# Kernel optimization log

Hardware: AMD Instinct MI355X
Metric: run time of the kernel (lower is better)

Reference implementation:

```python
import jax, jax.numpy as jnp
import numpy as np


def setup_inputs() -> dict:
    key = jax.random.key(0)
    k1, k2 = jax.random.split(key)
    x = jax.random.normal(k1, (4, 1, 16384), dtype=jnp.float32)  # [B, C, T]
    # dictionary initialized uniform(-1, 1) as in nn.Parameter(...).uniform_(-1, 1)
    d = jax.random.uniform(k2, (256, 1, 256), dtype=jnp.float32, minval=-1.0, maxval=1.0)  # [A, C, K]
    return {"x": x, "d": d, "n_iterations": 16}


def reference(x, d, n_iterations):
    B, C, T = x.shape
    A, _, K = d.shape
    pad = K // 2
    # normalize each atom over (channels, atom_size) dims, i.e. d_normalization_dims=(-1,-2)
    norms = jnp.linalg.norm(d.reshape(A, -1), axis=-1)
    dn = d / (norms[:, None, None] + 1e-12)

    # work in a padded domain so conv output position == start index in padded residual
    rp = jnp.pad(x, ((0, 0), (0, 0), (pad, pad)))        # residual, [B, C, T+2*pad]
    recon = jnp.zeros_like(rp)                            # accumulated reconstruction
    Tout = T + 2 * pad - K + 1                            # conv output length

    def step(carry, _):
        rp, recon = carry
        # cross-correlation of residual with every atom: [B, A, Tout]
        fm = jax.lax.conv_general_dilated(
            rp, dn, window_strides=(1,), padding='VALID',
            dimension_numbers=('NCH', 'OIH', 'NCH'))
        flat = fm.reshape(B, A * Tout)
        idx = jnp.argmax(flat, axis=-1)                   # signed max, per batch item
        val = jnp.take_along_axis(flat, idx[:, None], axis=-1)[:, 0]
        atom_idx = idx // Tout
        pos = idx % Tout                                  # start index in padded domain
        atoms = dn[atom_idx] * val[:, None, None]         # [B, C, K]

        def upd(r, rec, a, p):
            seg = jax.lax.dynamic_slice(r, (0, p), (C, K))
            r2 = jax.lax.dynamic_update_slice(r, seg - a, (0, p))
            segr = jax.lax.dynamic_slice(rec, (0, p), (C, K))
            rec2 = jax.lax.dynamic_update_slice(rec, segr + a, (0, p))
            return r2, rec2

        rp2, recon2 = jax.vmap(upd)(rp, recon, atoms, pos)
        return (rp2, recon2), None

    (rp, recon), _ = jax.lax.scan(step, (rp, recon), None, length=n_iterations)
    # crop padding -> reconstruction with same shape as x
    return recon[:, :, pad:pad + T]
```

## Files before the change

kernel.cpp:

```cpp
#include <hip/hip_runtime.h>
#include <math.h>

#define B    4
#define T    16384
#define A    256
#define K    256
#define PAD  128
#define TP   (T + 2*PAD)
#define TOUT (TP - K + 1)
#define ITERS 16
#define CHUNK 512
#define NCHUNK 33
#define NCP  36
#define TILE 2048
#define NTILE 9
#define NBLK 512
#define BPB2 128
#define HBASE 8192
#define RPSTORE 8448
#define RPN 8704
#define NGRP 8
#define SUBSTRIDE 32
#define BARSTRIDE (NGRP*SUBSTRIDE)
#define DLDS 40960

#define TAP(acc, s0,s1,s2,s3, dq) { acc = fmaf(s0,(dq).x,acc); acc = fmaf(s1,(dq).y,acc); \
                                    acc = fmaf(s2,(dq).z,acc); acc = fmaf(s3,(dq).w,acc); }

typedef unsigned long long u64;

__device__ __forceinline__ void wave_amax(float& bv, int& bi) {
    #pragma unroll
    for (int off = 32; off; off >>= 1) {
        float ov = __shfl_down(bv, off);
        int   oi = __shfl_down(bi, off);
        if (ov > bv || (ov == bv && oi < bi)) { bv = ov; bi = oi; }
    }
}

struct KSmem {
    float  rp[RPN];
    float4 dn4[4][64];
    float  chv[4][34];
    int    chi[4][34];
    float  wv[16]; int wi[16];
    float  fv; int fi;
};

__device__ __forceinline__ void gbar_sub(unsigned* sub, int r, unsigned gen16, int tid) {
    __syncthreads();
    if (tid == 0)
        __hip_atomic_fetch_add(&sub[(r >> 4)*SUBSTRIDE], 1u,
                               __ATOMIC_RELEASE, __HIP_MEMORY_SCOPE_AGENT);
    if (tid < 64) {
        for (;;) {
            unsigned ok = 1;
            if (tid < NGRP)
                ok = (__hip_atomic_load(&sub[tid*SUBSTRIDE], __ATOMIC_RELAXED,
                                        __HIP_MEMORY_SCOPE_AGENT) >= gen16);
            if (__all((int)ok)) break;
            __builtin_amdgcn_s_sleep(4);
        }
    }
    __syncthreads();
    __builtin_amdgcn_fence(__ATOMIC_ACQUIRE, "agent");
}

__device__ void chunks_update(KSmem& sm, int baseF, int cA, int cB, int aBase, int tid) {
    const int lane = tid & 63, w = tid >> 6;
    const int grp = tid >> 7;
    const int cg = grp ? cB : cA;
    const int lt = cg*512 + (tid & 127)*4;
    float c0[4] = {0,0,0,0}, c1[4] = {0,0,0,0}, c2[4] = {0,0,0,0}, c3[4] = {0,0,0,0};
    if (cg >= 0) {
        const float4* srp4 = (const float4*)sm.rp;
        int ol4 = (lt - baseF) >> 2;
        float4 p = srp4[ol4];
        #pragma unroll 4
        for (int kq = 0; kq < 64; kq++) {
            float4 d0 = sm.dn4[0][kq];
            float4 d1 = sm.dn4[1][kq];
            float4 d2 = sm.dn4[2][kq];
            float4 d3 = sm.dn4[3][kq];
            float4 pn = srp4[ol4 + kq + 1];
            TAP(c0[0], p.x,p.y,p.z,p.w, d0); TAP(c0[1], p.y,p.z,p.w,pn.x, d0);
            TAP(c0[2], p.z,p.w,pn.x,pn.y, d0); TAP(c0[3], p.w,pn.x,pn.y,pn.z, d0);
            TAP(c1[0], p.x,p.y,p.z,p.w, d1); TAP(c1[1], p.y,p.z,p.w,pn.x, d1);
            TAP(c1[2], p.z,p.w,pn.x,pn.y, d1); TAP(c1[3], p.w,pn.x,pn.y,pn.z, d1);
            TAP(c2[0], p.x,p.y,p.z,p.w, d2); TAP(c2[1], p.y,p.z,p.w,pn.x, d2);
            TAP(c2[2], p.z,p.w,pn.x,pn.y, d2); TAP(c2[3], p.w,pn.x,pn.y,pn.z, d2);
            TAP(c3[0], p.x,p.y,p.z,p.w, d3); TAP(c3[1], p.y,p.z,p.w,pn.x, d3);
            TAP(c3[2], p.z,p.w,pn.x,pn.y, d3); TAP(c3[3], p.w,pn.x,pn.y,pn.z, d3);
            p = pn;
        }
    }
    float bv0 = -INFINITY, bv1 = -INFINITY, bv2 = -INFINITY, bv3 = -INFINITY;
    int bi0 = 0x7fffffff, bi1 = 0x7fffffff, bi2 = 0x7fffffff, bi3 = 0x7fffffff;
    if (cg >= 0) {
        #pragma unroll
        for (int j = 0; j < 4; j++) {
            int t = lt + j;
            if (t < TOUT) {
                if (c0[j] > bv0) { bv0 = c0[j]; bi0 = (aBase+0)*TOUT + t; }
                if (c1[j] > bv1) { bv1 = c1[j]; bi1 = (aBase+1)*TOUT + t; }
                if (c2[j] > bv2) { bv2 = c2[j]; bi2 = (aBase+2)*TOUT + t; }
                if (c3[j] > bv3) { bv3 = c3[j]; bi3 = (aBase+3)*TOUT + t; }
            }
        }
    }
    wave_amax(bv0, bi0); wave_amax(bv1, bi1); wave_amax(bv2, bi2); wave_amax(bv3, bi3);
    if (lane == 0) {
        sm.wv[0*4+w] = bv0; sm.wi[0*4+w] = bi0;
        sm.wv[1*4+w] = bv1; sm.wi[1*4+w] = bi1;
        sm.wv[2*4+w] = bv2; sm.wi[2*4+w] = bi2;
        sm.wv[3*4+w] = bv3; sm.wi[3*4+w] = bi3;
    }
    __syncthreads();
    if (tid < 8) {
        int a = tid >> 1, hh = tid & 1;
        int chunk = hh ? cB : cA;
        if (chunk >= 0) {
            float v0 = sm.wv[a*4 + 2*hh];   int i0 = sm.wi[a*4 + 2*hh];
            float v1 = sm.wv[a*4 + 2*hh+1]; int i1 = sm.wi[a*4 + 2*hh+1];
            if (v1 > v0 || (v1 == v0 && i1 < i0)) { v0 = v1; i0 = i1; }
            sm.chv[a][chunk] = v0; sm.chi[a][chunk] = i0;
        }
    }
    __syncthreads();
}

__device__ __forceinline__ void slot_write(KSmem& sm, u64* wp, int gen, int h, int tid) {
    const int lane = tid & 63, w = tid >> 6;
    int cstart = h ? 16 : 0, nch = h ? 17 : 16;
    float bv = -INFINITY; int bi = 0x7fffffff;
    if (lane < nch) { bv = sm.chv[w][cstart + lane]; bi = sm.chi[w][cstart + lane]; }
    wave_amax(bv, bi);
    if (lane == 0) { sm.wv[8+w] = bv; sm.wi[8+w] = bi; }
    __syncthreads();
    if (tid == 0) {
        float v = sm.wv[8]; int i = sm.wi[8];
        #pragma unroll
        for (int j = 1; j < 4; j++)
            if (sm.wv[8+j] > v || (sm.wv[8+j] == v && sm.wi[8+j] < i)) { v = sm.wv[8+j]; i = sm.wi[8+j]; }
        u64 e = ((u64)(unsigned)(gen + 1) << 56)
              | ((u64)__float_as_uint(v) << 24)
              | (u64)(unsigned)i;
        __hip_atomic_store(wp, e, __ATOMIC_RELAXED, __HIP_MEMORY_SCOPE_AGENT);
    }
}

__device__ __forceinline__ void pick_poll(KSmem& sm, const u64* sl, int gen, int tid) {
    const int lane = tid & 63, w = tid >> 6;
    float v = -INFINITY; int i = 0x7fffffff;
    if (tid < BPB2) {
        const u64* p = sl + tid;
        u64 e;
        for (;;) {
            e = __hip_atomic_load(p, __ATOMIC_RELAXED, __HIP_MEMORY_SCOPE_AGENT);
            if ((unsigned)(e >> 56) == (unsigned)(gen + 1)) break;
            __builtin_amdgcn_s_sleep(1);
        }
        v = __uint_as_float((unsigned)((e >> 24) & 0xFFFFFFFFull));
        i = (int)(e & 0x7FFFFF);
    }
    if (w < 2) {
        wave_amax(v, i);
        if (lane == 0) { sm.wv[w] = v; sm.wi[w] = i; }
    }
    __syncthreads();
    if (tid == 0) {
        float bv = sm.wv[0]; int bi = sm.wi[0];
        if (sm.wv[1] > bv || (sm.wv[1] == bv && sm.wi[1] < bi)) { bv = sm.wv[1]; bi = sm.wi[1]; }
        sm.fv = bv; sm.fi = bi;
    }
    __syncthreads();
}

__global__ void __launch_bounds__(256, 2)
k_coop(const float* __restrict__ x, const float* __restrict__ d, float* __restrict__ out,
       float* __restrict__ dn, u64* __restrict__ slots, unsigned* __restrict__ bar) {
    extern __shared__ char raw[];
    KSmem& sm = *(KSmem*)raw;
    const int bid = blockIdx.x, tid = threadIdx.x;
    const int b = bid >> 7, r = bid & 127;
    const int h = r >> 6, a0 = r & 63;
    const int lane = tid & 63, w = tid >> 6;
    const int baseF = h * HBASE;
    const int cstart = h ? 16 : 0, cend = h ? 33 : 16;
    u64* slotsb = slots + (size_t)b*2*BPB2;
    unsigned* sub = bar + b*BARSTRIDE;

    {
        const float4* x4 = (const float4*)(x + (size_t)b*T);
        float4* rp4w = (float4*)sm.rp;
        int b4 = baseF >> 2;
        for (int i = tid; i < RPN/4; i += 256) {
            int g4 = b4 + i;
            float4 v = {0.f,0.f,0.f,0.f};
            if (i < RPSTORE/4 && g4 >= PAD/4 && g4 < (PAD+T)/4) v = x4[g4 - PAD/4];
            rp4w[i] = v;
        }
    }
    #pragma unroll
    for (int s = 0; s < 4; s++) {
        int atom = a0*4 + s;
        float v = d[atom*K + tid];
        float sq = v*v;
        #pragma unroll
        for (int off = 32; off; off >>= 1) sq += __shfl_down(sq, off);
        if (lane == 0) sm.wv[w] = sq;
        __syncthreads();
        float norm = sqrtf(sm.wv[0] + sm.wv[1] + sm.wv[2] + sm.wv[3]) + 1e-12f;
        float nv = v / norm;
        ((float*)&sm.dn4[s][0])[tid] = nv;
        dn[atom*K + tid] = nv;
        __syncthreads();
    }
    {
        int npass = h ? 9 : 8;
        for (int p = 0; p < npass; p++) {
            int ca = cstart + 2*p;
            int cb2 = (ca + 1 < cend) ? ca + 1 : -1;
            chunks_update(sm, baseF, ca, cb2, a0*4, tid);
        }
    }
    slot_write(sm, slotsb + 0*BPB2 + r, 0, h, tid);
    gbar_sub(sub, r, 16u, tid);

    for (int it = 0; it < ITERS-1; it++) {
        pick_poll(sm, slotsb + (it & 1)*BPB2, it, tid);
        float val = sm.fv; int idx = sm.fi;
        int atom = idx / TOUT, pos = idx - atom*TOUT;
        float ds = dn[atom*K + tid];
        int li = pos + tid - baseF;
        if (li >= 0 && li < RPSTORE) sm.rp[li] -= val * ds;
        __syncthreads();
        int lo = pos - (K-1); if (lo < 0) lo = 0;
        int g0 = lo >> 9, g1 = g0 + 1;
        bool in0 = (g0 >= cstart && g0 < cend);
        bool in1 = (g1 >= cstart && g1 < cend);
        int ca = in0 ? g0 : (in1 ? g1 : -1);
        int cb2 = (in0 && in1) ? g1 : -1;
        if (ca >= 0) chunks_update(sm, baseF, ca, cb2, a0*4, tid);
        slot_write(sm, slotsb + ((it+1) & 1)*BPB2 + r, it+1, h, tid);
    }
    if (a0 == 0) {
        pick_poll(sm, slotsb + ((ITERS-1) & 1)*BPB2, ITERS-1, tid);
        float val = sm.fv; int idx = sm.fi;
        int atom = idx / TOUT, pos = idx - atom*TOUT;
        float ds = dn[atom*K + tid];
        int li = pos + tid - baseF;
        if (li >= 0 && li < RPSTORE) sm.rp[li] -= val * ds;
        __syncthreads();
        int o_lo4 = h ? (HBASE - PAD)/4 : 0;
        int o_hi4 = h ? T/4 : (HBASE - PAD)/4;
        const float4* xb4 = (const float4*)(x + (size_t)b*T);
        float4* o4 = (float4*)(out + (size_t)b*T);
        for (int i4 = o_lo4 + tid; i4 < o_hi4; i4 += 256) {
            float4 xv = xb4[i4];
            float4 rv = *(const float4*)&sm.rp[i4*4 + PAD - baseF];
            float4 ov; ov.x = xv.x - rv.x; ov.y = xv.y - rv.y;
            ov.z = xv.z - rv.z; ov.w = xv.w - rv.w;
            o4[i4] = ov;
        }
    }
}

struct Smem {
    float rp[TILE + K + 16];
    float dnA[K];
    float dnB[K];
    float dnsel[K];
    float wv[16]; int wi[16];
    float fv; int fi;
};

__device__ __forceinline__ void dev_norm(int a0, int tid, const float* __restrict__ d,
                                         float* __restrict__ dn, Smem& sm) {
    int lane = tid & 63, w = tid >> 6;
    #pragma unroll
    for (int s = 0; s < 2; s++) {
        int atom = a0*2 + s;
        float v = d[atom*K + tid];
        float sq = v*v;
        #pragma unroll
        for (int off = 32; off; off >>= 1) sq += __shfl_down(sq, off);
        if (lane == 0) sm.wv[w] = sq;
        __syncthreads();
        float norm = sqrtf(sm.wv[0] + sm.wv[1] + sm.wv[2] + sm.wv[3]) + 1e-12f;
        dn[atom*K + tid] = v / norm;
        __syncthreads();
    }
}

__device__ __forceinline__ void dev_init(int a0, int b, int tid, const float* __restrict__ x,
                                         float* __restrict__ rp, float* __restrict__ recon) {
    int i = a0*256 + tid;
    if (i < TP) {
        float v = (i >= PAD && i < PAD + T) ? x[b*T + (i - PAD)] : 0.f;
        rp[(size_t)b*TP + i] = v;
        recon[(size_t)b*TP + i] = 0.f;
    }
}

__device__ void dev_conv(int a0, int b, int tid, const float* __restrict__ rp,
                         const float* __restrict__ dn,
                         float* __restrict__ segval, int* __restrict__ segidx,
                         float* __restrict__ abv, int* __restrict__ abi, Smem& sm) {
    const int aA = a0*2, aB = a0*2 + 1;
    const int lane = tid & 63, w = tid >> 6;
    sm.dnA[tid] = dn[aA*K + tid];
    sm.dnB[tid] = dn[aB*K + tid];
    const float4* rp4 = (const float4*)(rp + (size_t)b*TP);

    for (int tile = 0; tile < NTILE; tile++) {
        int t0 = tile * TILE;
        __syncthreads();
        float4* s4 = (float4*)sm.rp;
        for (int i = tid; i < 580; i += 256) {
            int g = t0/4 + i;
            float4 v = {0.f,0.f,0.f,0.f};
            if (g*4 < TP) v = rp4[g];
            s4[i] = v;
        }
        __syncthreads();
        const float4* srp4 = (const float4*)sm.rp;
        const float4* dA4  = (const float4*)sm.dnA;
        const float4* dB4  = (const float4*)sm.dnB;
        float accA0[4] = {0,0,0,0}, accA1[4] = {0,0,0,0};
        float accB0[4] = {0,0,0,0}, accB1[4] = {0,0,0,0};
        float4 p = srp4[tid];
        float4 q = srp4[tid + 256];
        #pragma unroll 4
        for (int kq = 0; kq < 64; kq++) {
            float4 dA = dA4[kq];
            float4 dB = dB4[kq];
            float4 pn = srp4[tid + kq + 1];
            float4 qn = srp4[tid + 256 + kq + 1];
            TAP(accA0[0], p.x,p.y,p.z,p.w, dA); TAP(accA0[1], p.y,p.z,p.w,pn.x, dA);
            TAP(accA0[2], p.z,p.w,pn.x,pn.y, dA); TAP(accA0[3], p.w,pn.x,pn.y,pn.z, dA);
            TAP(accB0[0], p.x,p.y,p.z,p.w, dB); TAP(accB0[1], p.y,p.z,p.w,pn.x, dB);
            TAP(accB0[2], p.z,p.w,pn.x,pn.y, dB); TAP(accB0[3], p.w,pn.x,pn.y,pn.z, dB);
            TAP(accA1[0], q.x,q.y,q.z,q.w, dA); TAP(accA1[1], q.y,q.z,q.w,qn.x, dA);
            TAP(accA1[2], q.z,q.w,qn.x,qn.y, dA); TAP(accA1[3], q.w,qn.x,qn.y,qn.z, dA);
            TAP(accB1[0], q.x,q.y,q.z,q.w, dB); TAP(accB1[1], q.y,q.z,q.w,qn.x, dB);
            TAP(accB1[2], q.z,q.w,qn.x,qn.y, dB); TAP(accB1[3], q.w,qn.x,qn.y,qn.z, dB);
            p = pn; q = qn;
        }
        int lt = tid * 4;
        float bvA0 = -INFINITY, bvA1 = -INFINITY, bvB0 = -INFINITY, bvB1 = -INFINITY;
        int biA0 = 0x7fffffff, biA1 = 0x7fffffff, biB0 = 0x7fffffff, biB1 = 0x7fffffff;
        #pragma unroll
        for (int j = 0; j < 4; j++) {
            int t = t0 + lt + j;
            if (t < TOUT) {
                if (accA0[j] > bvA0) { bvA0 = accA0[j]; biA0 = aA*TOUT + t; }
                if (accB0[j] > bvB0) { bvB0 = accB0[j]; biB0 = aB*TOUT + t; }
            }
            int t1 = t0 + 1024 + lt + j;
            if (t1 < TOUT) {
                if (accA1[j] > bvA1) { bvA1 = accA1[j]; biA1 = aA*TOUT + t1; }
                if (accB1[j] > bvB1) { bvB1 = accB1[j]; biB1 = aB*TOUT + t1; }
            }
        }
        wave_amax(bvA0, biA0); wave_amax(bvA1, biA1);
        wave_amax(bvB0, biB0); wave_amax(bvB1, biB1);
        if (lane == 0) {
            sm.wv[w]    = bvA0; sm.wi[w]    = biA0;
            sm.wv[4+w]  = bvA1; sm.wi[4+w]  = biA1;
            sm.wv[8+w]  = bvB0; sm.wi[8+w]  = biB0;
            sm.wv[12+w] = bvB1; sm.wi[12+w] = biB1;
        }
        __syncthreads();
        if (tid < 4) {
            float v0 = sm.wv[2*tid];   int i0 = sm.wi[2*tid];
            float v1 = sm.wv[2*tid+1]; int i1 = sm.wi[2*tid+1];
            if (v1 > v0 || (v1 == v0 && i1 < i0)) { v0 = v1; i0 = i1; }
            int chunk = tile*4 + tid;
            if (chunk < NCHUNK) {
                segval[((size_t)b*A + aA)*NCP + chunk] = v0;
                segidx[((size_t)b*A + aA)*NCP + chunk] = i0;
            }
        } else if (tid >= 64 && tid < 68) {
            int c = tid - 64;
            float v0 = sm.wv[8+2*c];   int i0 = sm.wi[8+2*c];
            float v1 = sm.wv[8+2*c+1]; int i1 = sm.wi[8+2*c+1];
            if (v1 > v0 || (v1 == v0 && i1 < i0)) { v0 = v1; i0 = i1; }
            int chunk = tile*4 + c;
            if (chunk < NCHUNK) {
                segval[((size_t)b*A + aB)*NCP + chunk] = v0;
                segidx[((size_t)b*A + aB)*NCP + chunk] = i0;
            }
        }
    }
    __syncthreads();
    if (w < 2) {
        int atom = (w == 0) ? aA : aB;
        float bv = -INFINITY; int bi = 0x7fffffff;
        if (lane < NCHUNK) {
            bv = segval[((size_t)b*A + atom)*NCP + lane];
            bi = segidx[((size_t)b*A + atom)*NCP + lane];
        }
        wave_amax(bv, bi);
        if (lane == 0) { abv[b*A + atom] = bv; abi[b*A + atom] = bi; }
    }
}

__device__ void dev_iter(int a0, int b, int tid, int last,
                         const float* __restrict__ avc, const int* __restrict__ aic,
                         float* __restrict__ avn, int* __restrict__ ain,
                         const float* __restrict__ rin, float* __restrict__ rout,
                         float* __restrict__ recon, const float* __restrict__ dn,
                         float* __restrict__ segval, int* __restrict__ segidx, Smem& sm) {
    const int aA = a0*2, aB = a0*2 + 1;
    const int lane = tid & 63, w = tid >> 6;

    float bv0 = avc[b*A + tid]; int bi0 = aic[b*A + tid];
    const float4* rin4 = (const float4*)(rin + (size_t)b*TP);
    const int icopy = a0*256 + tid;
    const bool docopy = (!last) && (icopy < TP/4);
    float4 vcopy = {0.f,0.f,0.f,0.f};
    if (docopy) vcopy = rin4[icopy];
    sm.dnA[tid] = dn[aA*K + tid];
    sm.dnB[tid] = dn[aB*K + tid];

    {
        float bv = bv0; int bi = bi0;
        wave_amax(bv, bi);
        if (lane == 0) { sm.wv[w] = bv; sm.wi[w] = bi; }
        __syncthreads();
        if (tid == 0) {
            bv = sm.wv[0]; bi = sm.wi[0];
            for (int j = 1; j < 4; j++)
                if (sm.wv[j] > bv || (sm.wv[j] == bv && sm.wi[j] < bi)) { bv = sm.wv[j]; bi = sm.wi[j]; }
            sm.fv = bv; sm.fi = bi;
        }
        __syncthreads();
    }
    float val = sm.fv; int idx = sm.fi;
    int atom = idx / TOUT, pos = idx - atom*TOUT;
    sm.dnsel[tid] = dn[atom*K + tid];

    int lo = pos - (K-1); if (lo < 0) lo = 0;
    int c_lo = lo >> 9;
    int tbase = c_lo * CHUNK;

    if (!last) {
        float4* s4 = (float4*)sm.rp;
        for (int i = tid; i < 324; i += 256) {
            int g = tbase/4 + i;
            float4 v = {0.f,0.f,0.f,0.f};
            if (g*4 < TP) v = rin4[g];
            s4[i] = v;
        }
    }
    __syncthreads();
    if (docopy) {
        float4* rout4 = (float4*)(rout + (size_t)b*TP);
        float4 v = vcopy;
        int o = icopy*4 - pos;
        if (o > -4 && o < K) {
            if (o+0 >= 0 && o+0 < K) v.x -= val * sm.dnsel[o+0];
            if (o+1 >= 0 && o+1 < K) v.y -= val * sm.dnsel[o+1];
            if (o+2 >= 0 && o+2 < K) v.z -= val * sm.dnsel[o+2];
            if (o+3 >= 0 && o+3 < K) v.w -= val * sm.dnsel[o+3];
        }
        rout4[icopy] = v;
    }
    if (a0 == 0) {
        recon[(size_t)b*TP + pos + tid] += val * sm.dnsel[tid];
    }
    if (last) return;

    sm.rp[pos + tid - tbase] -= val * sm.dnsel[tid];
    __syncthreads();

    const float4* srp4 = (const float4*)sm.rp;
    const float4* dA4  = (const float4*)sm.dnA;
    const float4* dB4  = (const float4*)sm.dnB;
    float cA[4] = {0,0,0,0}, cB[4] = {0,0,0,0};
    float4 p = srp4[tid];
    #pragma unroll 4
    for (int kq = 0; kq < 64; kq++) {
        float4 dA = dA4[kq];
        float4 dB = dB4[kq];
        float4 pn = srp4[tid + kq + 1];
        TAP(cA[0], p.x,p.y,p.z,p.w, dA); TAP(cA[1], p.y,p.z,p.w,pn.x, dA);
        TAP(cA[2], p.z,p.w,pn.x,pn.y, dA); TAP(cA[3], p.w,pn.x,pn.y,pn.z, dA);
        TAP(cB[0], p.x,p.y,p.z,p.w, dB); TAP(cB[1], p.y,p.z,p.w,pn.x, dB);
        TAP(cB[2], p.z,p.w,pn.x,pn.y, dB); TAP(cB[3], p.w,pn.x,pn.y,pn.z, dB);
        p = pn;
    }
    int lt = tid * 4;
    float bvA = -INFINITY, bvB = -INFINITY;
    int biA = 0x7fffffff, biB = 0x7fffffff;
    #pragma unroll
    for (int j = 0; j < 4; j++) {
        int t = tbase + lt + j;
        if (t < TOUT) {
            if (cA[j] > bvA) { bvA = cA[j]; biA = aA*TOUT + t; }
            if (cB[j] > bvB) { bvB = cB[j]; biB = aB*TOUT + t; }
        }
    }
    wave_amax(bvA, biA); wave_amax(bvB, biB);
    if (lane == 0) { sm.wv[w] = bvA; sm.wi[w] = biA; sm.wv[8+w] = bvB; sm.wi[8+w] = biB; }
    __syncthreads();
    if (tid < 2) {
        float v0 = sm.wv[2*tid];   int i0 = sm.wi[2*tid];
        float v1 = sm.wv[2*tid+1]; int i1 = sm.wi[2*tid+1];
        if (v1 > v0 || (v1 == v0 && i1 < i0)) { v0 = v1; i0 = i1; }
        int chunk = c_lo + tid;
        if (chunk < NCHUNK) {
            segval[((size_t)b*A + aA)*NCP + chunk] = v0;
            segidx[((size_t)b*A + aA)*NCP + chunk] = i0;
        }
    } else if (tid >= 64 && tid < 66) {
        int c = tid - 64;
        float v0 = sm.wv[8+2*c];   int i0 = sm.wi[8+2*c];
        float v1 = sm.wv[8+2*c+1]; int i1 = sm.wi[8+2*c+1];
        if (v1 > v0 || (v1 == v0 && i1 < i0)) { v0 = v1; i0 = i1; }
        int chunk = c_lo + c;
        if (chunk < NCHUNK) {
            segval[((size_t)b*A + aB)*NCP + chunk] = v0;
            segidx[((size_t)b*A + aB)*NCP + chunk] = i0;
        }
    }
    __syncthreads();
    if (w < 2) {
        int at = (w == 0) ? aA : aB;
        float bv = -INFINITY; int bi = 0x7fffffff;
        if (lane < NCHUNK) {
            bv = segval[((size_t)b*A + at)*NCP + lane];
            bi = segidx[((size_t)b*A + at)*NCP + lane];
        }
        wave_amax(bv, bi);
        if (lane == 0) { avn[b*A + at] = bv; ain[b*A + at] = bi; }
    }
}

__global__ void __launch_bounds__(256) k_f_norm_init(const float* x, const float* d,
                                                     float* dn, float* rp0, float* recon) {
    __shared__ Smem sm;
    dev_norm(blockIdx.x & 127, threadIdx.x, d, dn, sm);
    dev_init(blockIdx.x & 127, blockIdx.x >> 7, threadIdx.x, x, rp0, recon);
}
__global__ void __launch_bounds__(256, 2) k_f_conv(const float* rp, const float* dn,
                                                   float* segval, int* segidx,
                                                   float* abv, int* abi) {
    __shared__ Smem sm;
    dev_conv(blockIdx.x & 127, blockIdx.x >> 7, threadIdx.x, rp, dn, segval, segidx, abv, abi, sm);
}
__global__ void __launch_bounds__(256, 2) k_f_iter(int last,
                                                   const float* avc, const int* aic,
                                                   float* avn, int* ain,
                                                   const float* rin, float* rout,
                                                   float* recon, const float* dn,
                                                   float* segval, int* segidx) {
    __shared__ Smem sm;
    dev_iter(blockIdx.x & 127, blockIdx.x >> 7, threadIdx.x, last,
             avc, aic, avn, ain, rin, rout, recon, dn, segval, segidx, sm);
}
__global__ void k_f_out(const float* recon, float* out) {
    int i = blockIdx.x * blockDim.x + threadIdx.x;
    if (i >= B*T) return;
    int b = i / T, t = i - b*T;
    out[i] = recon[(size_t)b*TP + PAD + t];
}

extern "C" void kernel_launch(void* const* d_in, const int* in_sizes, int n_in,
                              void* d_out, int out_size, void* d_ws, size_t ws_size,
                              hipStream_t stream) {
    const float* x = (const float*)d_in[0];
    const float* d = (const float*)d_in[1];
    float* out = (float*)d_out;

    float* ws     = (float*)d_ws;
    float* dn     = ws;
    float* rp0    = dn  + (size_t)A*K;
    float* rp1    = rp0 + (size_t)B*TP;
    float* recon  = rp1 + (size_t)B*TP;
    float* segval = recon + (size_t)B*TP;
    int*   segidx = (int*)(segval + (size_t)B*A*NCP);
    float* abv0   = (float*)(segidx + (size_t)B*A*NCP);
    float* abv1   = abv0 + (size_t)B*2*A;
    int*   abi0   = (int*)(abv1 + (size_t)B*2*A);
    int*   abi1   = abi0 + (size_t)B*2*A;
    unsigned* bar = (unsigned*)(abi1 + (size_t)B*2*A);
    u64*  slots   = (u64*)(bar + (size_t)B*BARSTRIDE);

    (void)hipFuncSetAttribute((const void*)k_coop,
                              hipFuncAttributeMaxDynamicSharedMemorySize, DLDS);
    int nb = 0, ncu = 0;
    hipError_t e1 = hipOccupancyMaxActiveBlocksPerMultiprocessor(&nb, (const void*)k_coop,
                                                                 256, DLDS);
    hipError_t e2 = hipDeviceGetAttribute(&ncu, hipDeviceAttributeMultiprocessorCount, 0);
    bool coop = (e1 == hipSuccess && e2 == hipSuccess && nb > 0 && ncu > 0 &&
                 (long)nb * ncu >= NBLK);
    if (coop) {
        (void)hipMemsetAsync(bar, 0, B*BARSTRIDE*sizeof(unsigned), stream);
        (void)hipMemsetAsync(slots, 0xFF, (size_t)B*2*BPB2*sizeof(u64), stream);
        hipLaunchKernelGGL(k_coop, dim3(NBLK), dim3(256), DLDS, stream,
                           x, d, out, dn, slots, bar);
        return;
    }
    k_f_norm_init<<<NBLK, 256, 0, stream>>>(x, d, dn, rp0, recon);
    k_f_conv<<<NBLK, 256, 0, stream>>>(rp0, dn, segval, segidx, abv0, abi0);
    float* rbuf[2] = {rp0, rp1};
    float* av[2]   = {abv0, abv1};
    int*   ai[2]   = {abi0, abi1};
    for (int it = 0; it < ITERS; it++) {
        k_f_iter<<<NBLK, 256, 0, stream>>>(it == ITERS-1 ? 1 : 0,
                                           av[it & 1], ai[it & 1],
                                           av[(it + 1) & 1], ai[(it + 1) & 1],
                                           rbuf[it & 1], rbuf[(it + 1) & 1],
                                           recon, dn, segval, segidx);
    }
    k_f_out<<<(B*T + 255)/256, 256, 0, stream>>>(recon, out);
}
```

Baseline: 517.0 us.

## Replace per-block slot polling with grouped atomic-max argmax and arrival counters

Each block now folds its local best value and index into an order-preserving 64-bit key and does an atomic fetch_max into one of 8 group slots, then bumps a per-group arrival counter. Readers poll 8 counters and 8 group slots instead of 128 per-block slots, which shrinks polling traffic and the final reduction to a short shuffle. The generation is encoded in the high bits and slots are double-buffered by parity. Costs are atomic contention on shared slots and an explicit vmcnt wait between the max and the counter increment.

Result: no change. 517.0 us (-0.0%).

```diff
diff --git a/kernel.cpp b/kernel.cpp
--- a/kernel.cpp
+++ b/kernel.cpp
@@ -22,6 +22,8 @@
 #define NGRP 8
 #define SUBSTRIDE 32
 #define BARSTRIDE (NGRP*SUBSTRIDE)
+#define GSTRIDE 16
+#define GPAR (NGRP*GSTRIDE)
 #define DLDS 40960
 
 #define TAP(acc, s0,s1,s2,s3, dq) { acc = fmaf(s0,(dq).x,acc); acc = fmaf(s1,(dq).y,acc); \
@@ -129,7 +131,8 @@
     __syncthreads();
 }
 
-__device__ __forceinline__ void slot_write(KSmem& sm, u64* wp, int gen, int h, int tid) {
+__device__ __forceinline__ void publish(KSmem& sm, u64* gslot, unsigned* gcnt,
+                                        int gen, int h, int tid) {
     const int lane = tid & 63, w = tid >> 6;
     int cstart = h ? 16 : 0, nch = h ? 17 : 16;
     float bv = -INFINITY; int bi = 0x7fffffff;
@@ -142,43 +145,56 @@
         #pragma unroll
         for (int j = 1; j < 4; j++)
             if (sm.wv[8+j] > v || (sm.wv[8+j] == v && sm.wi[8+j] < i)) { v = sm.wv[8+j]; i = sm.wi[8+j]; }
-        u64 e = ((u64)(unsigned)(gen + 1) << 56)
-              | ((u64)__float_as_uint(v) << 24)
-              | (u64)(unsigned)i;
-        __hip_atomic_store(wp, e, __ATOMIC_RELAXED, __HIP_MEMORY_SCOPE_AGENT);
-    }
-}
-
-__device__ __forceinline__ void pick_poll(KSmem& sm, const u64* sl, int gen, int tid) {
-    const int lane = tid & 63, w = tid >> 6;
-    float v = -INFINITY; int i = 0x7fffffff;
-    if (tid < BPB2) {
-        const u64* p = sl + tid;
-        u64 e;
+        unsigned s = __float_as_uint(v);
+        unsigned key = (s & 0x80000000u) ? ~s : (s | 0x80000000u);
+        u64 e = ((u64)(unsigned)gen << 55) | ((u64)key << 23)
+              | (u64)(unsigned)(0x7FFFFF - i);
+        __hip_atomic_fetch_max(gslot, e, __ATOMIC_RELAXED, __HIP_MEMORY_SCOPE_AGENT);
+        asm volatile("s_waitcnt vmcnt(0)" ::: "memory");
+        __hip_atomic_fetch_add(gcnt, 1u, __ATOMIC_RELAXED, __HIP_MEMORY_SCOPE_AGENT);
+    }
+}
+
+__device__ __forceinline__ void pick(KSmem& sm, const u64* gparity,
+                                     const unsigned* cntb, int gen, int tid) {
+    const int lane = tid & 63;
+    if (tid < 64) {
         for (;;) {
-            e = __hip_atomic_load(p, __ATOMIC_RELAXED, __HIP_MEMORY_SCOPE_AGENT);
-            if ((unsigned)(e >> 56) == (unsigned)(gen + 1)) break;
-            __builtin_amdgcn_s_sleep(1);
-        }
-        v = __uint_as_float((unsigned)((e >> 24) & 0xFFFFFFFFull));
-        i = (int)(e & 0x7FFFFF);
-    }
-    if (w < 2) {
-        wave_amax(v, i);
-        if (lane == 0) { sm.wv[w] = v; sm.wi[w] = i; }
-    }
-    __syncthreads();
-    if (tid == 0) {
-        float bv = sm.wv[0]; int bi = sm.wi[0];
-        if (sm.wv[1] > bv || (sm.wv[1] == bv && sm.wi[1] < bi)) { bv = sm.wv[1]; bi = sm.wi[1]; }
-        sm.fv = bv; sm.fi = bi;
+            unsigned ok = 1;
+            if (lane < NGRP)
+                ok = (__hip_atomic_load(&cntb[lane*SUBSTRIDE], __ATOMIC_RELAXED,
+                                        __HIP_MEMORY_SCOPE_AGENT) >= (unsigned)gen*16u);
+            if (__all((int)ok)) break;
+            __builtin_amdgcn_s_sleep(2);
+        }
+        u64 e = 0;
+        if (lane < NGRP) {
+            const u64* p = gparity + lane*GSTRIDE;
+            for (;;) {
+                e = __hip_atomic_load(p, __ATOMIC_RELAXED, __HIP_MEMORY_SCOPE_AGENT);
+                if ((unsigned)(e >> 55) == (unsigned)gen) break;
+                __builtin_amdgcn_s_sleep(1);
+            }
+        }
+        #pragma unroll
+        for (int off = 4; off; off >>= 1) {
+            u64 o = __shfl_down(e, off);
+            if (lane < NGRP && o > e) e = o;
+        }
+        if (lane == 0) {
+            unsigned key = (unsigned)((e >> 23) & 0xFFFFFFFFull);
+            unsigned s = (key & 0x80000000u) ? (key ^ 0x80000000u) : ~key;
+            sm.fv = __uint_as_float(s);
+            sm.fi = 0x7FFFFF - (int)(e & 0x7FFFFF);
+        }
     }
     __syncthreads();
 }
 
 __global__ void __launch_bounds__(256, 2)
 k_coop(const float* __restrict__ x, const float* __restrict__ d, float* __restrict__ out,
-       float* __restrict__ dn, u64* __restrict__ slots, unsigned* __restrict__ bar) {
+       float* __restrict__ dn, u64* __restrict__ gmax,
+       unsigned* __restrict__ cnt, unsigned* __restrict__ fbar) {
     extern __shared__ char raw[];
     KSmem& sm = *(KSmem*)raw;
     const int bid = blockIdx.x, tid = threadIdx.x;
@@ -187,8 +203,10 @@
     const int lane = tid & 63, w = tid >> 6;
     const int baseF = h * HBASE;
     const int cstart = h ? 16 : 0, cend = h ? 33 : 16;
-    u64* slotsb = slots + (size_t)b*2*BPB2;
-    unsigned* sub = bar + b*BARSTRIDE;
+    const int grp = r >> 4;
+    u64* gmaxb = gmax + (size_t)b*2*GPAR;
+    unsigned* cntb = cnt + b*BARSTRIDE;
+    unsigned* fbarb = fbar + b*BARSTRIDE;
 
     {
         const float4* x4 = (const float4*)(x + (size_t)b*T);
@@ -224,11 +242,12 @@
             chunks_update(sm, baseF, ca, cb2, a0*4, tid);
         }
     }
-    slot_write(sm, slotsb + 0*BPB2 + r, 0, h, tid);
-    gbar_sub(sub, r, 16u, tid);
+    int gen = 1;
+    publish(sm, gmaxb + (gen&1)*GPAR + grp*GSTRIDE, cntb + grp*SUBSTRIDE, gen, h, tid);
+    gbar_sub(fbarb, r, 16u, tid);
 
     for (int it = 0; it < ITERS-1; it++) {
-        pick_poll(sm, slotsb + (it & 1)*BPB2, it, tid);
+        pick(sm, gmaxb + (gen&1)*GPAR, cntb, gen, tid);
         float val = sm.fv; int idx = sm.fi;
         int atom = idx / TOUT, pos = idx - atom*TOUT;
         float ds = dn[atom*K + tid];
@@ -242,10 +261,12 @@
         int ca = in0 ? g0 : (in1 ? g1 : -1);
         int cb2 = (in0 && in1) ? g1 : -1;
         if (ca >= 0) chunks_update(sm, baseF, ca, cb2, a0*4, tid);
-        slot_write(sm, slotsb + ((it+1) & 1)*BPB2 + r, it+1, h, tid);
+        publish(sm, gmaxb + ((gen+1)&1)*GPAR + grp*GSTRIDE, cntb + grp*SUBSTRIDE,
+                gen+1, h, tid);
+        gen++;
     }
     if (a0 == 0) {
-        pick_poll(sm, slotsb + ((ITERS-1) & 1)*BPB2, ITERS-1, tid);
+        pick(sm, gmaxb + (gen&1)*GPAR, cntb, gen, tid);
         float val = sm.fv; int idx = sm.fi;
         int atom = idx / TOUT, pos = idx - atom*TOUT;
         float ds = dn[atom*K + tid];
@@ -585,8 +606,9 @@
     float* abv1   = abv0 + (size_t)B*2*A;
     int*   abi0   = (int*)(abv1 + (size_t)B*2*A);
     int*   abi1   = abi0 + (size_t)B*2*A;
-    unsigned* bar = (unsigned*)(abi1 + (size_t)B*2*A);
-    u64*  slots   = (u64*)(bar + (size_t)B*BARSTRIDE);
+    unsigned* cnt = (unsigned*)(abi1 + (size_t)B*2*A);
+    unsigned* fbar= cnt + (size_t)B*BARSTRIDE;
+    u64*  gmax    = (u64*)(fbar + (size_t)B*BARSTRIDE);
 
     (void)hipFuncSetAttribute((const void*)k_coop,
                               hipFuncAttributeMaxDynamicSharedMemorySize, DLDS);
@@ -597,10 +619,10 @@
     bool coop = (e1 == hipSuccess && e2 == hipSuccess && nb > 0 && ncu > 0 &&
                  (long)nb * ncu >= NBLK);
     if (coop) {
-        (void)hipMemsetAsync(bar, 0, B*BARSTRIDE*sizeof(unsigned), stream);
-        (void)hipMemsetAsync(slots, 0xFF, (size_t)B*2*BPB2*sizeof(u64), stream);
+        size_t zbytes = (size_t)B*BARSTRIDE*4*2 + (size_t)B*2*GPAR*8;
+        (void)hipMemsetAsync(cnt, 0, zbytes, stream);
         hipLaunchKernelGGL(k_coop, dim3(NBLK), dim3(256), DLDS, stream,
-                           x, d, out, dn, slots, bar);
+                           x, d, out, dn, gmax, cnt, fbar);
         return;
     }
     k_f_norm_init<<<NBLK, 256, 0, stream>>>(x, d, dn, rp0, recon);
```
